# Kernel tuning notes

Measured on AMD Instinct MI355X. Metric: run time of the kernel, lower is better.

The kernel has to match this reference:

```python
import jax, jax.numpy as jnp
import numpy as np

N_QUBITS = 10
BATCH = 16384
Q_DEPTH = 2


def _apply_1q_shared(state, U, q):
    # state: [B, 2, 2, ..., 2]; U: [2, 2] complex, acting on wire q
    state = jnp.moveaxis(state, 1 + q, -1)
    state = jnp.einsum('b...i,ji->b...j', state, U)
    return jnp.moveaxis(state, -1, 1 + q)


def _apply_ry_batched(state, angles, q):
    # per-sample RY(angle) on wire q; angles: [B] float
    c = jnp.cos(angles * 0.5).astype(jnp.complex64)
    s = jnp.sin(angles * 0.5).astype(jnp.complex64)
    U = jnp.stack([jnp.stack([c, -s], -1), jnp.stack([s, c], -1)], -2)  # [B,2,2]
    state = jnp.moveaxis(state, 1 + q, -1)
    state = jnp.einsum('b...i,bji->b...j', state, U)
    return jnp.moveaxis(state, -1, 1 + q)


def _rot_matrix(phi, theta, omega):
    # PennyLane Rot = RZ(omega) @ RY(theta) @ RZ(phi)
    c = jnp.cos(theta * 0.5)
    s = jnp.sin(theta * 0.5)
    m00 = jnp.exp(-0.5j * (phi + omega)) * c
    m01 = -jnp.exp(0.5j * (phi - omega)) * s
    m10 = jnp.exp(-0.5j * (phi - omega)) * s
    m11 = jnp.exp(0.5j * (phi + omega)) * c
    return jnp.stack([jnp.stack([m00, m01]), jnp.stack([m10, m11])]).astype(jnp.complex64)


def _apply_cnot(state, c, t):
    st = jnp.moveaxis(state, (1 + c, 1 + t), (1, 2))  # [B, ctrl, tgt, ...]
    st = jnp.stack([st[:, 0], st[:, 1, ::-1]], axis=1)  # flip target where ctrl=1
    return jnp.moveaxis(st, (1, 2), (1 + c, 1 + t))


def setup_inputs() -> dict:
    key = jax.random.key(0)
    k1, k2 = jax.random.split(key)
    x = jax.random.uniform(k1, (BATCH, N_QUBITS), dtype=jnp.float32) * np.pi
    q_weights = 0.01 * jax.random.normal(k2, (Q_DEPTH, N_QUBITS, 3), dtype=jnp.float32)
    return {"x": x, "q_weights": q_weights}


def reference(x, q_weights) -> jnp.ndarray:
    B, n = x.shape
    L = q_weights.shape[0]
    # |0...0> statevector, batched: [B] + [2]*n (axis q <-> wire q, wire 0 most significant)
    state = jnp.zeros((B, 2 ** n), jnp.complex64).at[:, 0].set(1.0)
    state = state.reshape((B,) + (2,) * n)
    # AngleEmbedding(rotation='Y')
    for q in range(n):
        state = _apply_ry_batched(state, x[:, q], q)
    # StronglyEntanglingLayers: Rot on each wire, then ring of CNOTs with range (l % (n-1)) + 1
    for l in range(L):
        for q in range(n):
            U = _rot_matrix(q_weights[l, q, 0], q_weights[l, q, 1], q_weights[l, q, 2])
            state = _apply_1q_shared(state, U, q)
        r = (l % (n - 1)) + 1
        for q in range(n):
            state = _apply_cnot(state, q, (q + r) % n)
    probs = jnp.abs(state.reshape(B, 2 ** n)) ** 2  # [B, 2^n]
    bits = (np.arange(2 ** n)[:, None] >> (n - 1 - np.arange(n))[None, :]) & 1
    signs = jnp.asarray(1.0 - 2.0 * bits, jnp.float32)  # [2^n, n], PauliZ eigenvalues
    return (probs @ signs).astype(jnp.float32)  # [B, n] expvals
```

## Files before the change

kernel.cpp:

```cpp
#include <hip/hip_runtime.h>

#define DEVINL __device__ __forceinline__

typedef _Float16 h2_t __attribute__((ext_vector_type(2)));

struct GC { int laneXor, regXor, rowL, rowR; };
struct Circ { GC g[20]; int sgnL[10], sgnR[10]; };

constexpr Circ build_circ() {
    Circ c{};
    unsigned A[10] = {};
    for (int i = 0; i < 10; ++i) A[i] = 1u << i;
    for (int w = 0; w < 10; ++w) {
        int pos = 9 - w;
        unsigned m = 1u << pos;
        c.g[w] = GC{ int(m >> 4), int(m & 15u), int(m >> 4), int(m & 15u) };
    }
    for (int q = 0; q < 10; ++q) { int pc = 9 - q, pt = 9 - ((q + 1) % 10); A[pt] ^= A[pc]; }
    unsigned M[10] = {}, Inv[10] = {};
    for (int i = 0; i < 10; ++i) { M[i] = A[i]; Inv[i] = 1u << i; }
    for (int col = 0; col < 10; ++col) {
        int piv = col;
        while (!((M[piv] >> col) & 1u)) ++piv;
        unsigned tm = M[col]; M[col] = M[piv]; M[piv] = tm;
        unsigned ti = Inv[col]; Inv[col] = Inv[piv]; Inv[piv] = ti;
        for (int r = 0; r < 10; ++r)
            if (r != col && ((M[r] >> col) & 1u)) { M[r] ^= M[col]; Inv[r] ^= Inv[col]; }
    }
    for (int w = 0; w < 10; ++w) {
        int pos = 9 - w;
        unsigned m = 0;
        for (int i = 0; i < 10; ++i) m |= ((Inv[i] >> pos) & 1u) << i;
        unsigned row = A[pos];
        c.g[10 + w] = GC{ int(m >> 4), int(m & 15u), int(row >> 4), int(row & 15u) };
    }
    for (int q = 0; q < 10; ++q) { int pc = 9 - q, pt = 9 - ((q + 2) % 10); A[pt] ^= A[pc]; }
    for (int q = 0; q < 10; ++q) { unsigned row = A[9 - q]; c.sgnL[q] = int(row >> 4); c.sgnR[q] = int(row & 15u); }
    return c;
}

constexpr Circ CC = build_circ();

DEVINL float csign(float v, int s) {
    return __int_as_float(__float_as_int(v) ^ (s << 31));
}

DEVINL int pk(float a, float b) {
    return __builtin_bit_cast(int, __builtin_amdgcn_cvt_pkrtz(a, b));
}
DEVINL float fdot2(int p, int v, float acc) {
    return __builtin_amdgcn_fdot2(__builtin_bit_cast(h2_t, p), __builtin_bit_cast(h2_t, v), acc, false);
}

template<int XOR>
DEVINL int lxi(int x, int lane) {
    if constexpr (XOR == 1)      return __builtin_amdgcn_update_dpp(0, x, 0xB1, 0xF, 0xF, true);
    else if constexpr (XOR == 2) return __builtin_amdgcn_update_dpp(0, x, 0x4E, 0xF, 0xF, true);
    else if constexpr (XOR == 3) return __builtin_amdgcn_update_dpp(0, x, 0x1B, 0xF, 0xF, true);
    else if constexpr (XOR < 32) return __builtin_amdgcn_ds_swizzle(x, 0x1F | (XOR << 10));
    else                         return __builtin_amdgcn_ds_bpermute((lane ^ XOR) << 2, x);
}
template<int XOR>
DEVINL float lxf(float v, int lane) {
    return __int_as_float(lxi<XOR>(__float_as_int(v), lane));
}

template<int G>
DEVINL void gates(int (&a)[16], const int* smP, int lane) {
    if constexpr (G < 20) {
        constexpr GC gc = CC.g[G];
        int sL = __popc(unsigned(lane & gc.rowL)) & 1;
        int p1 = smP[G * 4 + 0] ^ (sL << 31);
        int p2 = smP[G * 4 + 1] ^ (sL << 15);
        int p3 = smP[G * 4 + 2] ^ (sL << 15);
        int p4 = smP[G * 4 + 3] ^ (sL << 31);
        int q1 = p1 ^ (int)0x80000000;
        int q2 = p2 ^ 0x8000;
        int q3 = p3 ^ 0x8000;
        int q4 = p4 ^ (int)0x80000000;
        int b_[16];
        if constexpr (gc.laneXor == 0) {
            #pragma unroll
            for (int r = 0; r < 16; ++r) b_[r] = a[r ^ gc.regXor];
        } else {
            #pragma unroll
            for (int r = 0; r < 16; ++r) b_[r] = lxi<gc.laneXor>(a[r ^ gc.regXor], lane);
        }
        #pragma unroll
        for (int r = 0; r < 16; ++r) {
            const int cR = __builtin_popcount(unsigned(gc.rowR & r)) & 1;
            float nr = fdot2(cR ? q1 : p1, a[r], fdot2(cR ? q2 : p2, b_[r], 0.f));
            float ni = fdot2(cR ? q3 : p3, a[r], fdot2(cR ? q4 : p4, b_[r], 0.f));
            a[r] = pk(nr, ni);
        }
        gates<G + 1>(a, smP, lane);
    }
}

__global__ __launch_bounds__(256) void qsim(const float* __restrict__ x,
                                            const float* __restrict__ qw,
                                            float* __restrict__ out, int B) {
    __shared__ float sm32[80];
    __shared__ int smP[80];
    {
        int g = threadIdx.x;
        if (g < 20) {
            float phi = qw[g * 3 + 0], th = qw[g * 3 + 1], om = qw[g * 3 + 2];
            float c = cosf(0.5f * th), s = sinf(0.5f * th);
            float apo = 0.5f * (phi + om), amo = 0.5f * (phi - om);
            float m0 =  cosf(apo) * c;
            float m1 = -sinf(apo) * c;
            float m2 = -cosf(amo) * s;
            float m3 = -sinf(amo) * s;
            sm32[g * 4 + 0] = m0; sm32[g * 4 + 1] = m1;
            sm32[g * 4 + 2] = m2; sm32[g * 4 + 3] = m3;
            smP[g * 4 + 0] = pk(m0, -m1);
            smP[g * 4 + 1] = pk(m2, -m3);
            smP[g * 4 + 2] = pk(m1,  m0);
            smP[g * 4 + 3] = pk(m3,  m2);
        }
    }
    __syncthreads();

    int lane = threadIdx.x & 63;
    int b = __builtin_amdgcn_readfirstlane(blockIdx.x * 4 + (threadIdx.x >> 6));
    if (b >= B) return;

    const float* xb = x + b * 10;
    float f0r[10], f0i[10], f1r[10], f1i[10];
    #pragma unroll
    for (int w = 0; w < 10; ++w) {
        float h = 0.5f * xb[w];
        float s = __sinf(h), c = __cosf(h);
        float m0 = sm32[w * 4 + 0], m1 = sm32[w * 4 + 1], m2 = sm32[w * 4 + 2], m3 = sm32[w * 4 + 3];
        f0r[w] =  m0 * c + m2 * s;
        f0i[w] =  m1 * c + m3 * s;
        f1r[w] = -m2 * c + m0 * s;
        f1i[w] =  m3 * c - m1 * s;
    }
    float lfr, lfi;
    {
        int bit = lane & 1;
        lfr = bit ? f1r[5] : f0r[5];
        lfi = bit ? f1i[5] : f0i[5];
    }
    #pragma unroll
    for (int jj = 1; jj < 6; ++jj) {
        int w = 5 - jj;
        int bit = (lane >> jj) & 1;
        float pr = bit ? f1r[w] : f0r[w];
        float pi = bit ? f1i[w] : f0i[w];
        float nr = lfr * pr - lfi * pi;
        float ni = lfr * pi + lfi * pr;
        lfr = nr; lfi = ni;
    }
    float t01r[4], t01i[4], t23r[4], t23i[4];
    #pragma unroll
    for (int v = 0; v < 4; ++v) {
        float ar9 = (v & 1) ? f1r[9] : f0r[9], ai9 = (v & 1) ? f1i[9] : f0i[9];
        float ar8 = (v >> 1) ? f1r[8] : f0r[8], ai8 = (v >> 1) ? f1i[8] : f0i[8];
        t01r[v] = ar9 * ar8 - ai9 * ai8;
        t01i[v] = ar9 * ai8 + ai9 * ar8;
        float ar7 = (v & 1) ? f1r[7] : f0r[7], ai7 = (v & 1) ? f1i[7] : f0i[7];
        float ar6 = (v >> 1) ? f1r[6] : f0r[6], ai6 = (v >> 1) ? f1i[6] : f0i[6];
        t23r[v] = ar7 * ar6 - ai7 * ai6;
        t23i[v] = ar7 * ai6 + ai7 * ar6;
    }
    float g4r[4], g4i[4];
    #pragma unroll
    for (int v = 0; v < 4; ++v) {
        g4r[v] = lfr * t01r[v] - lfi * t01i[v];
        g4i[v] = lfr * t01i[v] + lfi * t01r[v];
    }
    int a[16];
    #pragma unroll
    for (int r = 0; r < 16; ++r) {
        float ar = g4r[r & 3] * t23r[r >> 2] - g4i[r & 3] * t23i[r >> 2];
        float ai = g4r[r & 3] * t23i[r >> 2] + g4i[r & 3] * t23r[r >> 2];
        a[r] = pk(ar, ai);
    }

    gates<10>(a, smP, lane);

    float t[16];
    #pragma unroll
    for (int r = 0; r < 16; ++r) t[r] = fdot2(a[r], a[r], 0.f);
    #pragma unroll
    for (int bit = 1; bit < 16; bit <<= 1) {
        #pragma unroll
        for (int i = 0; i < 16; ++i) {
            if ((i & bit) == 0) {
                float u = t[i], v = t[i | bit];
                t[i] = u + v;
                t[i | bit] = u - v;
            }
        }
    }
    float e[10];
    #pragma unroll
    for (int q = 0; q < 10; ++q) {
        int sl = __popc(unsigned(lane & CC.sgnL[q])) & 1;
        e[q] = csign(t[CC.sgnR[q]], sl);
    }
    #pragma unroll
    for (int q = 0; q < 10; ++q) {
        e[q] += lxf<1>(e[q], lane);
        e[q] += lxf<2>(e[q], lane);
        e[q] += lxf<4>(e[q], lane);
        e[q] += lxf<8>(e[q], lane);
        e[q] += lxf<16>(e[q], lane);
        e[q] += lxf<32>(e[q], lane);
    }
    float v = e[0];
    #pragma unroll
    for (int q = 1; q < 10; ++q) v = (lane == q) ? e[q] : v;
    if (lane < 10) out[b * 10 + lane] = v;
}

extern "C" void kernel_launch(void* const* d_in, const int* in_sizes, int n_in,
                              void* d_out, int out_size, void* d_ws, size_t ws_size,
                              hipStream_t stream) {
    const float* x  = (const float*)d_in[0];
    const float* qw = (const float*)d_in[1];
    float* out = (float*)d_out;
    int B = in_sizes[0] / 10;
    int blocks = (B + 3) / 4;
    hipLaunchKernelGGL(qsim, dim3(blocks), dim3(256), 0, stream, x, qw, out, B);
}
```

Baseline: 99.08 us.

## Replace cross-lane gate exchanges with LDS permutation transposes between gate groups

Each layer's gates no longer use per-gate DPP or swizzle lane exchanges plus fp16 dot products. The statevector is now re-laid out through shared memory with precomputed GF(2) index maps, so that each group of wires sits in register bits, and the gates then run as fp32 register-local butterflies. The goal is to drop the lane-exchange traffic and pack/unpack work of twenty gates in favour of three scatter/gather passes through LDS. In exchange the kernel uses 32 KB of shared memory per block, which may lower occupancy, adds __syncthreads barriers, and out-of-range waves now run redundantly instead of returning early.

```diff
diff --git a/kernel.cpp b/kernel.cpp
--- a/kernel.cpp
+++ b/kernel.cpp
@@ -4,226 +4,304 @@
 
 typedef _Float16 h2_t __attribute__((ext_vector_type(2)));
 
-struct GC { int laneXor, regXor, rowL, rowR; };
-struct Circ { GC g[20]; int sgnL[10], sgnR[10]; };
-
-constexpr Circ build_circ() {
-    Circ c{};
-    unsigned A[10] = {};
-    for (int i = 0; i < 10; ++i) A[i] = 1u << i;
-    for (int w = 0; w < 10; ++w) {
-        int pos = 9 - w;
-        unsigned m = 1u << pos;
-        c.g[w] = GC{ int(m >> 4), int(m & 15u), int(m >> 4), int(m & 15u) };
+constexpr unsigned P1[10] = {9,8,7,6,5,4,3,2,1,0};
+constexpr unsigned P2[10] = {3,2,1,0,5,4,9,8,7,6};
+constexpr unsigned P3[10] = {5,4,9,8,7,6,3,2,1,0};
+
+struct Maps2 {
+  unsigned emb_j[6], emb_r[16];
+  unsigned s12_j[6], s12_r[16];
+  unsigned s23_j[6], s23_r[16];
+  unsigned rho_l[10], rho_r[10];
+  bool ok;
+};
+
+constexpr unsigned mulF2(const unsigned* R, unsigned v) {
+  unsigned o = 0;
+  for (int i = 0; i < 10; ++i) o |= unsigned(__builtin_popcount(R[i] & v) & 1) << i;
+  return o;
+}
+constexpr unsigned locP(const unsigned* P, unsigned L) {
+  unsigned s = 0;
+  for (int j = 0; j < 10; ++j) s |= ((L >> P[j]) & 1u) << j;
+  return s;
+}
+
+constexpr Maps2 build2() {
+  Maps2 M{};
+  unsigned C1[10], C2[10];
+  for (int i = 0; i < 10; ++i) { C1[i] = 1u << i; C2[i] = 1u << i; }
+  for (int q = 0; q < 10; ++q) C1[9 - ((q + 1) % 10)] ^= C1[9 - q];
+  for (int q = 0; q < 10; ++q) C2[9 - ((q + 2) % 10)] ^= C2[9 - q];
+
+  unsigned embc[10], c12[10], c23[10];
+  for (int j = 0; j < 10; ++j) embc[j] = locP(P1, mulF2(C1, 1u << j));
+  for (int j = 0; j < 10; ++j) c12[j]  = locP(P2, 1u << P1[j]);
+  for (int j = 0; j < 10; ++j) c23[j]  = locP(P3, 1u << P2[j]);
+
+  for (int jj = 0; jj < 6; ++jj) {
+    M.emb_j[jj] = embc[4 + jj];
+    M.s12_j[jj] = c12[4 + jj];
+    M.s23_j[jj] = c23[4 + jj];
+  }
+  for (int r = 0; r < 16; ++r) {
+    unsigned a = 0, b = 0, c = 0;
+    for (int k = 0; k < 4; ++k)
+      if ((r >> k) & 1) { a ^= embc[k]; b ^= c12[k]; c ^= c23[k]; }
+    M.emb_r[r] = a; M.s12_r[r] = b; M.s23_r[r] = c;
+  }
+  for (int q = 0; q < 10; ++q) {
+    unsigned row = C2[9 - q], rho = 0;
+    for (int j = 0; j < 10; ++j) rho |= ((row >> P3[j]) & 1u) << j;
+    M.rho_r[q] = rho & 15u;
+    M.rho_l[q] = rho >> 4;
+  }
+
+  bool ok = true;
+  ok = ok && (9 - P1[0] == 0) && (9 - P1[1] == 1) && (9 - P1[2] == 2) && (9 - P1[3] == 3);
+  ok = ok && (9 - P2[0] == 6) && (9 - P2[1] == 7) && (9 - P2[2] == 8) && (9 - P2[3] == 9);
+  ok = ok && (9 - P3[0] == 4) && (9 - P3[1] == 5);
+  for (int p = 0; p < 10; ++p) {
+    unsigned L = 1u << p;
+    unsigned s1 = locP(P1, L), s2 = 0;
+    for (int j = 0; j < 10; ++j) if ((s1 >> j) & 1u) s2 ^= c12[j];
+    ok = ok && (s2 == locP(P2, L));
+    unsigned t2 = locP(P2, L), t3 = 0;
+    for (int j = 0; j < 10; ++j) if ((t2 >> j) & 1u) t3 ^= c23[j];
+    ok = ok && (t3 == locP(P3, L));
+  }
+  for (int q = 0; q < 10; ++q) {
+    unsigned rho = M.rho_r[q] | (M.rho_l[q] << 4);
+    for (int j = 0; j < 10; ++j) {
+      unsigned b = 1u << P3[j];
+      unsigned cc = mulF2(C2, b);
+      ok = ok && (((cc >> (9 - q)) & 1u) == ((rho >> j) & 1u));
     }
-    for (int q = 0; q < 10; ++q) { int pc = 9 - q, pt = 9 - ((q + 1) % 10); A[pt] ^= A[pc]; }
-    unsigned M[10] = {}, Inv[10] = {};
-    for (int i = 0; i < 10; ++i) { M[i] = A[i]; Inv[i] = 1u << i; }
-    for (int col = 0; col < 10; ++col) {
-        int piv = col;
-        while (!((M[piv] >> col) & 1u)) ++piv;
-        unsigned tm = M[col]; M[col] = M[piv]; M[piv] = tm;
-        unsigned ti = Inv[col]; Inv[col] = Inv[piv]; Inv[piv] = ti;
-        for (int r = 0; r < 10; ++r)
-            if (r != col && ((M[r] >> col) & 1u)) { M[r] ^= M[col]; Inv[r] ^= Inv[col]; }
-    }
-    for (int w = 0; w < 10; ++w) {
-        int pos = 9 - w;
-        unsigned m = 0;
-        for (int i = 0; i < 10; ++i) m |= ((Inv[i] >> pos) & 1u) << i;
-        unsigned row = A[pos];
-        c.g[10 + w] = GC{ int(m >> 4), int(m & 15u), int(row >> 4), int(row & 15u) };
-    }
-    for (int q = 0; q < 10; ++q) { int pc = 9 - q, pt = 9 - ((q + 2) % 10); A[pt] ^= A[pc]; }
-    for (int q = 0; q < 10; ++q) { unsigned row = A[9 - q]; c.sgnL[q] = int(row >> 4); c.sgnR[q] = int(row & 15u); }
-    return c;
-}
-
-constexpr Circ CC = build_circ();
+  }
+  M.ok = ok;
+  return M;
+}
+
+constexpr Maps2 MM = build2();
+static_assert(MM.ok, "index-map self-check failed");
 
 DEVINL float csign(float v, int s) {
-    return __int_as_float(__float_as_int(v) ^ (s << 31));
-}
-
+  return __int_as_float(__float_as_int(v) ^ (s << 31));
+}
 DEVINL int pk(float a, float b) {
-    return __builtin_bit_cast(int, __builtin_amdgcn_cvt_pkrtz(a, b));
-}
-DEVINL float fdot2(int p, int v, float acc) {
-    return __builtin_amdgcn_fdot2(__builtin_bit_cast(h2_t, p), __builtin_bit_cast(h2_t, v), acc, false);
-}
-
-template<int XOR>
-DEVINL int lxi(int x, int lane) {
-    if constexpr (XOR == 1)      return __builtin_amdgcn_update_dpp(0, x, 0xB1, 0xF, 0xF, true);
-    else if constexpr (XOR == 2) return __builtin_amdgcn_update_dpp(0, x, 0x4E, 0xF, 0xF, true);
-    else if constexpr (XOR == 3) return __builtin_amdgcn_update_dpp(0, x, 0x1B, 0xF, 0xF, true);
-    else if constexpr (XOR < 32) return __builtin_amdgcn_ds_swizzle(x, 0x1F | (XOR << 10));
-    else                         return __builtin_amdgcn_ds_bpermute((lane ^ XOR) << 2, x);
+  return __builtin_bit_cast(int, __builtin_amdgcn_cvt_pkrtz(a, b));
 }
 template<int XOR>
 DEVINL float lxf(float v, int lane) {
-    return __int_as_float(lxi<XOR>(__float_as_int(v), lane));
-}
-
-template<int G>
-DEVINL void gates(int (&a)[16], const int* smP, int lane) {
-    if constexpr (G < 20) {
-        constexpr GC gc = CC.g[G];
-        int sL = __popc(unsigned(lane & gc.rowL)) & 1;
-        int p1 = smP[G * 4 + 0] ^ (sL << 31);
-        int p2 = smP[G * 4 + 1] ^ (sL << 15);
-        int p3 = smP[G * 4 + 2] ^ (sL << 15);
-        int p4 = smP[G * 4 + 3] ^ (sL << 31);
-        int q1 = p1 ^ (int)0x80000000;
-        int q2 = p2 ^ 0x8000;
-        int q3 = p3 ^ 0x8000;
-        int q4 = p4 ^ (int)0x80000000;
-        int b_[16];
-        if constexpr (gc.laneXor == 0) {
-            #pragma unroll
-            for (int r = 0; r < 16; ++r) b_[r] = a[r ^ gc.regXor];
-        } else {
-            #pragma unroll
-            for (int r = 0; r < 16; ++r) b_[r] = lxi<gc.laneXor>(a[r ^ gc.regXor], lane);
-        }
-        #pragma unroll
-        for (int r = 0; r < 16; ++r) {
-            const int cR = __builtin_popcount(unsigned(gc.rowR & r)) & 1;
-            float nr = fdot2(cR ? q1 : p1, a[r], fdot2(cR ? q2 : p2, b_[r], 0.f));
-            float ni = fdot2(cR ? q3 : p3, a[r], fdot2(cR ? q4 : p4, b_[r], 0.f));
-            a[r] = pk(nr, ni);
-        }
-        gates<G + 1>(a, smP, lane);
+  int x = __float_as_int(v); int r;
+  if constexpr (XOR == 1)      r = __builtin_amdgcn_update_dpp(0, x, 0xB1, 0xF, 0xF, true);
+  else if constexpr (XOR == 2) r = __builtin_amdgcn_update_dpp(0, x, 0x4E, 0xF, 0xF, true);
+  else if constexpr (XOR == 3) r = __builtin_amdgcn_update_dpp(0, x, 0x1B, 0xF, 0xF, true);
+  else if constexpr (XOR < 32) r = __builtin_amdgcn_ds_swizzle(x, 0x1F | (XOR << 10));
+  else                         r = __builtin_amdgcn_ds_bpermute((lane ^ XOR) << 2, x);
+  return __int_as_float(r);
+}
+
+template<int BIT>
+DEVINL void gate_bit(float (&ar)[16], float (&ai)[16], float m0, float m1, float m2, float m3) {
+  #pragma unroll
+  for (int r = 0; r < 16; ++r) {
+    if (!(r & (1 << BIT))) {
+      const int p = r | (1 << BIT);
+      float xr = ar[r], xi = ai[r], yr = ar[p], yi = ai[p];
+      ar[r] =  m0*xr - m1*xi + m2*yr - m3*yi;
+      ai[r] =  m1*xr + m0*xi + m3*yr + m2*yi;
+      ar[p] =  m0*yr + m1*yi - m2*xr - m3*xi;
+      ai[p] = -m1*yr + m0*yi + m3*xr - m2*xi;
     }
+  }
+}
+
+DEVINL void scatter16(const float (&ar)[16], const float (&ai)[16], int* buf,
+                      int lc, const unsigned (&cols)[16]) {
+  #pragma unroll
+  for (int r = 0; r < 16; ++r) buf[lc ^ (int)cols[r]] = pk(ar[r], ai[r]);
+}
+DEVINL void gather16(float (&ar)[16], float (&ai)[16], const int* buf, int lane) {
+  #pragma unroll
+  for (int v = 0; v < 4; ++v) {
+    int4 w4 = *(const int4*)(buf + lane * 16 + v * 4);
+    int vv[4] = {w4.x, w4.y, w4.z, w4.w};
+    #pragma unroll
+    for (int d = 0; d < 4; ++d) {
+      h2_t h = __builtin_bit_cast(h2_t, vv[d]);
+      ar[v*4+d] = (float)h.x;
+      ai[v*4+d] = (float)h.y;
+    }
+  }
 }
 
 __global__ __launch_bounds__(256) void qsim(const float* __restrict__ x,
                                             const float* __restrict__ qw,
                                             float* __restrict__ out, int B) {
-    __shared__ float sm32[80];
-    __shared__ int smP[80];
-    {
-        int g = threadIdx.x;
-        if (g < 20) {
-            float phi = qw[g * 3 + 0], th = qw[g * 3 + 1], om = qw[g * 3 + 2];
-            float c = cosf(0.5f * th), s = sinf(0.5f * th);
-            float apo = 0.5f * (phi + om), amo = 0.5f * (phi - om);
-            float m0 =  cosf(apo) * c;
-            float m1 = -sinf(apo) * c;
-            float m2 = -cosf(amo) * s;
-            float m3 = -sinf(amo) * s;
-            sm32[g * 4 + 0] = m0; sm32[g * 4 + 1] = m1;
-            sm32[g * 4 + 2] = m2; sm32[g * 4 + 3] = m3;
-            smP[g * 4 + 0] = pk(m0, -m1);
-            smP[g * 4 + 1] = pk(m2, -m3);
-            smP[g * 4 + 2] = pk(m1,  m0);
-            smP[g * 4 + 3] = pk(m3,  m2);
-        }
+  __shared__ __align__(16) float sm32[80];
+  __shared__ __align__(16) int bufA[4][1024];
+  __shared__ __align__(16) int bufB[4][1024];
+  int tid = threadIdx.x;
+  if (tid < 20) {
+    float phi = qw[tid*3+0], th = qw[tid*3+1], om = qw[tid*3+2];
+    float c = cosf(0.5f*th), s = sinf(0.5f*th);
+    float apo = 0.5f*(phi+om), amo = 0.5f*(phi-om);
+    sm32[tid*4+0] =  cosf(apo)*c;
+    sm32[tid*4+1] = -sinf(apo)*c;
+    sm32[tid*4+2] = -cosf(amo)*s;
+    sm32[tid*4+3] = -sinf(amo)*s;
+  }
+  __syncthreads();
+
+  int lane = tid & 63, wv = tid >> 6;
+  int bidx = __builtin_amdgcn_readfirstlane(blockIdx.x*4 + wv);
+  int bld = bidx < B ? bidx : (B - 1);
+
+  const float* xb = x + bld * 10;
+  float f0r[10], f0i[10], f1r[10], f1i[10];
+  #pragma unroll
+  for (int w = 0; w < 10; ++w) {
+    float h = 0.5f * xb[w];
+    float s = __sinf(h), c = __cosf(h);
+    float m0 = sm32[w*4+0], m1 = sm32[w*4+1], m2 = sm32[w*4+2], m3 = sm32[w*4+3];
+    f0r[w] =  m0*c + m2*s;
+    f0i[w] =  m1*c + m3*s;
+    f1r[w] = -m2*c + m0*s;
+    f1i[w] =  m3*c - m1*s;
+  }
+  float lfr, lfi;
+  {
+    int bit = lane & 1;
+    lfr = bit ? f1r[5] : f0r[5];
+    lfi = bit ? f1i[5] : f0i[5];
+  }
+  #pragma unroll
+  for (int jj = 1; jj < 6; ++jj) {
+    int w = 5 - jj;
+    int bit = (lane >> jj) & 1;
+    float pr = bit ? f1r[w] : f0r[w];
+    float pi = bit ? f1i[w] : f0i[w];
+    float nr = lfr*pr - lfi*pi;
+    float ni = lfr*pi + lfi*pr;
+    lfr = nr; lfi = ni;
+  }
+  float t01r[4], t01i[4], t23r[4], t23i[4];
+  #pragma unroll
+  for (int v = 0; v < 4; ++v) {
+    float ar9 = (v&1)? f1r[9]:f0r[9], ai9 = (v&1)? f1i[9]:f0i[9];
+    float ar8 = (v>>1)? f1r[8]:f0r[8], ai8 = (v>>1)? f1i[8]:f0i[8];
+    t01r[v] = ar9*ar8 - ai9*ai8;
+    t01i[v] = ar9*ai8 + ai9*ar8;
+    float ar7 = (v&1)? f1r[7]:f0r[7], ai7 = (v&1)? f1i[7]:f0i[7];
+    float ar6 = (v>>1)? f1r[6]:f0r[6], ai6 = (v>>1)? f1i[6]:f0i[6];
+    t23r[v] = ar7*ar6 - ai7*ai6;
+    t23i[v] = ar7*ai6 + ai7*ar6;
+  }
+  float g4r[4], g4i[4];
+  #pragma unroll
+  for (int v = 0; v < 4; ++v) {
+    g4r[v] = lfr*t01r[v] - lfi*t01i[v];
+    g4i[v] = lfr*t01i[v] + lfi*t01r[v];
+  }
+
+  int lcE = 0, lc12 = 0, lc23 = 0;
+  #pragma unroll
+  for (int jj = 0; jj < 6; ++jj) {
+    int bit = (lane >> jj) & 1;
+    lcE  ^= bit ? (int)MM.emb_j[jj] : 0;
+    lc12 ^= bit ? (int)MM.s12_j[jj] : 0;
+    lc23 ^= bit ? (int)MM.s23_j[jj] : 0;
+  }
+
+  #pragma unroll
+  for (int r = 0; r < 16; ++r) {
+    float er = g4r[r&3]*t23r[r>>2] - g4i[r&3]*t23i[r>>2];
+    float ei = g4r[r&3]*t23i[r>>2] + g4i[r&3]*t23r[r>>2];
+    bufA[wv][lcE ^ (int)MM.emb_r[r]] = pk(er, ei);
+  }
+  __syncthreads();
+
+  float ar[16], ai[16];
+  gather16(ar, ai, &bufA[wv][0], lane);
+
+  {
+    float4 c0 = *(const float4*)(sm32 + 10*4);
+    float4 c1 = *(const float4*)(sm32 + 11*4);
+    float4 c2 = *(const float4*)(sm32 + 12*4);
+    float4 c3 = *(const float4*)(sm32 + 13*4);
+    gate_bit<0>(ar, ai, c0.x, c0.y, c0.z, c0.w);
+    gate_bit<1>(ar, ai, c1.x, c1.y, c1.z, c1.w);
+    gate_bit<2>(ar, ai, c2.x, c2.y, c2.z, c2.w);
+    gate_bit<3>(ar, ai, c3.x, c3.y, c3.z, c3.w);
+  }
+  scatter16(ar, ai, &bufB[wv][0], lc12, MM.s12_r);
+  __syncthreads();
+  gather16(ar, ai, &bufB[wv][0], lane);
+
+  {
+    float4 c0 = *(const float4*)(sm32 + 16*4);
+    float4 c1 = *(const float4*)(sm32 + 17*4);
+    float4 c2 = *(const float4*)(sm32 + 18*4);
+    float4 c3 = *(const float4*)(sm32 + 19*4);
+    gate_bit<0>(ar, ai, c0.x, c0.y, c0.z, c0.w);
+    gate_bit<1>(ar, ai, c1.x, c1.y, c1.z, c1.w);
+    gate_bit<2>(ar, ai, c2.x, c2.y, c2.z, c2.w);
+    gate_bit<3>(ar, ai, c3.x, c3.y, c3.z, c3.w);
+  }
+  scatter16(ar, ai, &bufA[wv][0], lc23, MM.s23_r);
+  __syncthreads();
+  gather16(ar, ai, &bufA[wv][0], lane);
+
+  {
+    float4 c0 = *(const float4*)(sm32 + 14*4);
+    float4 c1 = *(const float4*)(sm32 + 15*4);
+    gate_bit<0>(ar, ai, c0.x, c0.y, c0.z, c0.w);
+    gate_bit<1>(ar, ai, c1.x, c1.y, c1.z, c1.w);
+  }
+
+  float t[16];
+  #pragma unroll
+  for (int r = 0; r < 16; ++r) t[r] = ar[r]*ar[r] + ai[r]*ai[r];
+  #pragma unroll
+  for (int bit = 1; bit < 16; bit <<= 1) {
+    #pragma unroll
+    for (int i = 0; i < 16; ++i) {
+      if ((i & bit) == 0) {
+        float u = t[i], v = t[i|bit];
+        t[i] = u + v;
+        t[i|bit] = u - v;
+      }
     }
-    __syncthreads();
-
-    int lane = threadIdx.x & 63;
-    int b = __builtin_amdgcn_readfirstlane(blockIdx.x * 4 + (threadIdx.x >> 6));
-    if (b >= B) return;
-
-    const float* xb = x + b * 10;
-    float f0r[10], f0i[10], f1r[10], f1i[10];
-    #pragma unroll
-    for (int w = 0; w < 10; ++w) {
-        float h = 0.5f * xb[w];
-        float s = __sinf(h), c = __cosf(h);
-        float m0 = sm32[w * 4 + 0], m1 = sm32[w * 4 + 1], m2 = sm32[w * 4 + 2], m3 = sm32[w * 4 + 3];
-        f0r[w] =  m0 * c + m2 * s;
-        f0i[w] =  m1 * c + m3 * s;
-        f1r[w] = -m2 * c + m0 * s;
-        f1i[w] =  m3 * c - m1 * s;
-    }
-    float lfr, lfi;
-    {
-        int bit = lane & 1;
-        lfr = bit ? f1r[5] : f0r[5];
-        lfi = bit ? f1i[5] : f0i[5];
-    }
-    #pragma unroll
-    for (int jj = 1; jj < 6; ++jj) {
-        int w = 5 - jj;
-        int bit = (lane >> jj) & 1;
-        float pr = bit ? f1r[w] : f0r[w];
-        float pi = bit ? f1i[w] : f0i[w];
-        float nr = lfr * pr - lfi * pi;
-        float ni = lfr * pi + lfi * pr;
-        lfr = nr; lfi = ni;
-    }
-    float t01r[4], t01i[4], t23r[4], t23i[4];
-    #pragma unroll
-    for (int v = 0; v < 4; ++v) {
-        float ar9 = (v & 1) ? f1r[9] : f0r[9], ai9 = (v & 1) ? f1i[9] : f0i[9];
-        float ar8 = (v >> 1) ? f1r[8] : f0r[8], ai8 = (v >> 1) ? f1i[8] : f0i[8];
-        t01r[v] = ar9 * ar8 - ai9 * ai8;
-        t01i[v] = ar9 * ai8 + ai9 * ar8;
-        float ar7 = (v & 1) ? f1r[7] : f0r[7], ai7 = (v & 1) ? f1i[7] : f0i[7];
-        float ar6 = (v >> 1) ? f1r[6] : f0r[6], ai6 = (v >> 1) ? f1i[6] : f0i[6];
-        t23r[v] = ar7 * ar6 - ai7 * ai6;
-        t23i[v] = ar7 * ai6 + ai7 * ar6;
-    }
-    float g4r[4], g4i[4];
-    #pragma unroll
-    for (int v = 0; v < 4; ++v) {
-        g4r[v] = lfr * t01r[v] - lfi * t01i[v];
-        g4i[v] = lfr * t01i[v] + lfi * t01r[v];
-    }
-    int a[16];
-    #pragma unroll
-    for (int r = 0; r < 16; ++r) {
-        float ar = g4r[r & 3] * t23r[r >> 2] - g4i[r & 3] * t23i[r >> 2];
-        float ai = g4r[r & 3] * t23i[r >> 2] + g4i[r & 3] * t23r[r >> 2];
-        a[r] = pk(ar, ai);
-    }
-
-    gates<10>(a, smP, lane);
-
-    float t[16];
-    #pragma unroll
-    for (int r = 0; r < 16; ++r) t[r] = fdot2(a[r], a[r], 0.f);
-    #pragma unroll
-    for (int bit = 1; bit < 16; bit <<= 1) {
-        #pragma unroll
-        for (int i = 0; i < 16; ++i) {
-            if ((i & bit) == 0) {
-                float u = t[i], v = t[i | bit];
-                t[i] = u + v;
-                t[i | bit] = u - v;
-            }
-        }
-    }
-    float e[10];
-    #pragma unroll
-    for (int q = 0; q < 10; ++q) {
-        int sl = __popc(unsigned(lane & CC.sgnL[q])) & 1;
-        e[q] = csign(t[CC.sgnR[q]], sl);
-    }
-    #pragma unroll
-    for (int q = 0; q < 10; ++q) {
-        e[q] += lxf<1>(e[q], lane);
-        e[q] += lxf<2>(e[q], lane);
-        e[q] += lxf<4>(e[q], lane);
-        e[q] += lxf<8>(e[q], lane);
-        e[q] += lxf<16>(e[q], lane);
-        e[q] += lxf<32>(e[q], lane);
-    }
-    float v = e[0];
-    #pragma unroll
-    for (int q = 1; q < 10; ++q) v = (lane == q) ? e[q] : v;
-    if (lane < 10) out[b * 10 + lane] = v;
+  }
+  float e[10];
+  #pragma unroll
+  for (int q = 0; q < 10; ++q) {
+    int sl = __popc(unsigned(lane & (int)MM.rho_l[q])) & 1;
+    e[q] = csign(t[MM.rho_r[q]], sl);
+  }
+  #pragma unroll
+  for (int q = 0; q < 10; ++q) {
+    e[q] += lxf<1>(e[q], lane);
+    e[q] += lxf<2>(e[q], lane);
+    e[q] += lxf<4>(e[q], lane);
+    e[q] += lxf<8>(e[q], lane);
+    e[q] += lxf<16>(e[q], lane);
+    e[q] += lxf<32>(e[q], lane);
+  }
+  float v = e[0];
+  #pragma unroll
+  for (int q = 1; q < 10; ++q) v = (lane == q) ? e[q] : v;
+  if (bidx < B && lane < 10) out[bidx * 10 + lane] = v;
 }
 
 extern "C" void kernel_launch(void* const* d_in, const int* in_sizes, int n_in,
                               void* d_out, int out_size, void* d_ws, size_t ws_size,
                               hipStream_t stream) {
-    const float* x  = (const float*)d_in[0];
-    const float* qw = (const float*)d_in[1];
-    float* out = (float*)d_out;
-    int B = in_sizes[0] / 10;
-    int blocks = (B + 3) / 4;
-    hipLaunchKernelGGL(qsim, dim3(blocks), dim3(256), 0, stream, x, qw, out, B);
-}
+  const float* x  = (const float*)d_in[0];
+  const float* qw = (const float*)d_in[1];
+  float* out = (float*)d_out;
+  int B = in_sizes[0] / 10;
+  int blocks = (B + 3) / 4;
+  hipLaunchKernelGGL(qsim, dim3(blocks), dim3(256), 0, stream, x, qw, out, B);
+}
```

Result: slower. 118.5 us (+19.6%).
